# Kernel optimization log

Hardware: AMD Instinct MI355X
Metric: run time of the kernel (lower is better)

The kernel has to match this reference:

```python
import jax, jax.numpy as jnp
import numpy as np

B, T, C, H = 2, 2048, 1024, 16


def setup_inputs() -> dict:
    key = jax.random.key(0)
    ks = jax.random.split(key, 5)
    s = 0.02
    x = jax.random.normal(ks[0], (B, T, C), dtype=jnp.float32)
    # causal mask, shape [1, 1, T, T], 1 = attend, 0 = masked
    att_mask = jnp.tril(jnp.ones((T, T), dtype=jnp.int32))[None, None, :, :]
    w_kqv = jax.random.normal(ks[1], (C, 3 * C), dtype=jnp.float32) * s
    b_kqv = jax.random.normal(ks[2], (3 * C,), dtype=jnp.float32) * s
    w_proj = jax.random.normal(ks[3], (C, C), dtype=jnp.float32) * s
    b_proj = jax.random.normal(ks[4], (C,), dtype=jnp.float32) * s
    return {"x": x, "att_mask": att_mask, "w_kqv": w_kqv, "b_kqv": b_kqv,
            "w_proj": w_proj, "b_proj": b_proj, "n_head": H}


def reference(x, att_mask, w_kqv, b_kqv, w_proj, b_proj, n_head):
    b, t, c = x.shape
    hd = c // n_head
    # mixed kqv projection, then per-head chunks of 3*hd split as (k, q, v)
    kqv = (x @ w_kqv + b_kqv).reshape(b, t, n_head, 3 * hd)
    k, q, v = jnp.split(kqv, 3, axis=-1)            # each [b, t, h, hd]
    k = k.transpose(0, 2, 1, 3)                     # [b, h, t, hd]
    q = q.transpose(0, 2, 1, 3)
    v = v.transpose(0, 2, 1, 3)
    scale = 1.0 / np.sqrt(hd).astype(np.float32)
    att = jnp.einsum('bhqd,bhkd->bhqk', q, k) * scale
    att = jnp.where(att_mask[:, :, :t, :t] == 0, jnp.float32(-jnp.inf), att)
    att = jax.nn.softmax(att, axis=-1)
    y = jnp.einsum('bhqk,bhkd->bhqd', att, v)       # [b, h, t, hd]
    y = y.transpose(0, 2, 1, 3).reshape(b, t, c)
    return y @ w_proj + b_proj
```

## Files before the change

### kernel.cpp

```cpp
#include <hip/hip_runtime.h>
#include <hip/hip_bf16.h>

#define NB 2
#define NT 2048
#define NC 1024
#define NH 16
#define HD 64

typedef __attribute__((ext_vector_type(8))) short short8;
typedef __attribute__((ext_vector_type(4))) short short4_;
typedef __attribute__((ext_vector_type(4))) float f32x4;
typedef unsigned short u16;

__device__ __forceinline__ u16 f2bf(float x) {
  union { float f; unsigned u; } c; c.f = x;
  unsigned r = (c.u + 0x7fffu + ((c.u >> 16) & 1u)) >> 16;
  return (u16)r;
}


__global__ void cvt_x_kernel(const float* __restrict__ in, u16* __restrict__ out, int n) {
  int i = (blockIdx.x * blockDim.x + threadIdx.x) * 4;
  if (i < n) {
    float4 v = *(const float4*)(in + i);
    short4_ o;
    o.x = (short)f2bf(v.x); o.y = (short)f2bf(v.y);
    o.z = (short)f2bf(v.z); o.w = (short)f2bf(v.w);
    *(short4_*)(out + i) = o;
  }
}

__global__ void transpose_w_kernel(const float* __restrict__ in, u16* __restrict__ out,
                                   int K, int N) {
  __shared__ float tile[32][33];
  int k0 = blockIdx.x * 32, n0 = blockIdx.y * 32;
  int tx = threadIdx.x, ty = threadIdx.y;
  for (int r = ty; r < 32; r += 8)
    tile[r][tx] = in[(size_t)(k0 + r) * N + n0 + tx];
  __syncthreads();
  for (int r = ty; r < 32; r += 8)
    out[(size_t)(n0 + r) * K + k0 + tx] = f2bf(tile[tx][r]);
}


__global__ __launch_bounds__(256, 2) void gemm_kqv(
    const u16* __restrict__ A, const u16* __restrict__ Bt,
    const float* __restrict__ bias,
    u16* __restrict__ o_k, u16* __restrict__ o_q, u16* __restrict__ o_vt,
    int M, int N, int K) {
  __shared__ u16 As[128 * 32];
  __shared__ u16 Bs[128 * 32];
  __shared__ u16 Cs[128 * 128];
  int tid = threadIdx.x;
  int w = tid >> 6, l = tid & 63;
  int wr = w >> 1, wc = w & 1;
  int lr = l & 15, lk = l >> 4;
  int bm = blockIdx.x, bn = blockIdx.y;

  const u16* Ab = A + (size_t)bm * 128 * K;
  const u16* Bb = Bt + (size_t)bn * 128 * K;

  f32x4 acc[4][4];
#pragma unroll
  for (int m = 0; m < 4; m++)
#pragma unroll
    for (int n = 0; n < 4; n++) acc[m][n] = (f32x4){0.f, 0.f, 0.f, 0.f};

  for (int ks = 0; ks < K; ks += 32) {
    __syncthreads();
#pragma unroll
    for (int it = 0; it < 2; ++it) {
      int chunk = it * 256 + tid;
      int r = chunk >> 2, kg = chunk & 3;
      const u16* ga = Ab + (size_t)r * K + ks + kg * 8;
      const u16* gb = Bb + (size_t)r * K + ks + kg * 8;
      u16* la = As + (size_t)(it * 256 + w * 64) * 8;
      u16* lb = Bs + (size_t)(it * 256 + w * 64) * 8;
      __builtin_amdgcn_global_load_lds((const __attribute__((address_space(1))) void*)ga,
                                       (__attribute__((address_space(3))) void*)la, 16, 0, 0);
      __builtin_amdgcn_global_load_lds((const __attribute__((address_space(1))) void*)gb,
                                       (__attribute__((address_space(3))) void*)lb, 16, 0, 0);
    }
    __syncthreads();
    short8 a[4], b[4];
#pragma unroll
    for (int m = 0; m < 4; m++)
      a[m] = *(const short8*)(As + (size_t)(wr * 64 + m * 16 + lr) * 32 + lk * 8);
#pragma unroll
    for (int n = 0; n < 4; n++)
      b[n] = *(const short8*)(Bs + (size_t)(wc * 64 + n * 16 + lr) * 32 + lk * 8);
#pragma unroll
    for (int m = 0; m < 4; m++)
#pragma unroll
      for (int n = 0; n < 4; n++)
        acc[m][n] = __builtin_amdgcn_mfma_f32_16x16x32_bf16(a[m], b[n], acc[m][n], 0, 0, 0);
  }

#pragma unroll
  for (int n = 0; n < 4; n++) {
    int col = wc * 64 + n * 16 + lr;
    float bv = bias[bn * 128 + col];
#pragma unroll
    for (int m = 0; m < 4; m++) {
#pragma unroll
      for (int j = 0; j < 4; j++) {
        int row = wr * 64 + m * 16 + lk * 4 + j;
        int bo = (row * 256 + col * 2) ^ (((row >> 2) & 3) << 5);
        *(u16*)((char*)Cs + bo) = f2bf(acc[m][n][j] + bv);
      }
    }
  }
  __syncthreads();
#pragma unroll
  for (int i = 0; i < 8; i++) {
    int idx = i * 256 + tid;
    int row = idx >> 4, g = idx & 15;
    int gcol0 = bn * 128 + g * 8;
    unsigned head = (unsigned)gcol0 / 192u;
    int rem = gcol0 - (int)head * 192;
    int typ = rem >> 6, d0 = rem & 63;
    if (typ < 2) {
      int bo = (row * 256 + g * 16) ^ (((row >> 2) & 3) << 5);
      short8 val = *(const short8*)((const char*)Cs + bo);
      int grow = bm * 128 + row;
      int b_ = grow >> 11, t_ = grow & (NT - 1);
      size_t base = ((size_t)(b_ * NH + head) * NT + t_) * HD + d0;
      if (typ == 0) *(short8*)(o_k + base) = val;
      else          *(short8*)(o_q + base) = val;
    }
  }
  for (int i = tid; i < 128 * 16; i += 256) {
    int c = i >> 4, rg = i & 15;
    int gcol = bn * 128 + c;
    unsigned head = (unsigned)gcol / 192u;
    int rem = gcol - (int)head * 192;
    if (rem >= 128) {
      int d = rem - 128;
      short8 val;
#pragma unroll
      for (int k = 0; k < 8; k++) {
        int row = rg * 8 + k;
        int bo = (row * 256 + c * 2) ^ (((row >> 2) & 3) << 5);
        val[k] = *(const u16*)((const char*)Cs + bo);
      }
      int grow0 = bm * 128 + rg * 8;
      int b_ = grow0 >> 11, t0 = grow0 & (NT - 1);
      *(short8*)(o_vt + ((size_t)(b_ * NH + head) * HD + d) * NT + t0) = val;
    }
  }
}


__global__ __launch_bounds__(256, 2) void gemm_out(
    const u16* __restrict__ A, const u16* __restrict__ Bt,
    const float* __restrict__ bias, float* __restrict__ o_f, int M, int N, int K) {
  __shared__ u16 As[128 * 32];
  __shared__ u16 Bs[64 * 32];
  int tid = threadIdx.x;
  int w = tid >> 6, l = tid & 63;
  int wr = w >> 1, wc = w & 1;
  int lr = l & 15, lk = l >> 4;
  int bm = blockIdx.x, bn = blockIdx.y;

  const u16* Ab = A + (size_t)bm * 128 * K;
  const u16* Bb = Bt + (size_t)bn * 64 * K;

  f32x4 acc[4][2];
#pragma unroll
  for (int m = 0; m < 4; m++)
#pragma unroll
    for (int n = 0; n < 2; n++) acc[m][n] = (f32x4){0.f, 0.f, 0.f, 0.f};

  for (int ks = 0; ks < K; ks += 32) {
    __syncthreads();
#pragma unroll
    for (int it = 0; it < 2; ++it) {
      int chunk = it * 256 + tid;
      int r = chunk >> 2, kg = chunk & 3;
      const u16* ga = Ab + (size_t)r * K + ks + kg * 8;
      u16* la = As + (size_t)(it * 256 + w * 64) * 8;
      __builtin_amdgcn_global_load_lds((const __attribute__((address_space(1))) void*)ga,
                                       (__attribute__((address_space(3))) void*)la, 16, 0, 0);
    }
    {
      int r = tid >> 2, kg = tid & 3;
      const u16* gb = Bb + (size_t)r * K + ks + kg * 8;
      u16* lb = Bs + (size_t)(w * 64) * 8;
      __builtin_amdgcn_global_load_lds((const __attribute__((address_space(1))) void*)gb,
                                       (__attribute__((address_space(3))) void*)lb, 16, 0, 0);
    }
    __syncthreads();
    short8 a[4], b[2];
#pragma unroll
    for (int m = 0; m < 4; m++)
      a[m] = *(const short8*)(As + (size_t)(wr * 64 + m * 16 + lr) * 32 + lk * 8);
#pragma unroll
    for (int n = 0; n < 2; n++)
      b[n] = *(const short8*)(Bs + (size_t)(wc * 32 + n * 16 + lr) * 32 + lk * 8);
#pragma unroll
    for (int m = 0; m < 4; m++)
#pragma unroll
      for (int n = 0; n < 2; n++)
        acc[m][n] = __builtin_amdgcn_mfma_f32_16x16x32_bf16(a[m], b[n], acc[m][n], 0, 0, 0);
  }

#pragma unroll
  for (int m = 0; m < 4; m++) {
    int gm0 = bm * 128 + wr * 64 + m * 16 + lk * 4;
#pragma unroll
    for (int n = 0; n < 2; n++) {
      int gn = bn * 64 + wc * 32 + n * 16 + lr;
      float bv = bias[gn];
#pragma unroll
      for (int j = 0; j < 4; j++)
        o_f[(size_t)(gm0 + j) * N + gn] = acc[m][n][j] + bv;
    }
  }
}


#define SMSCALE 0.1803368801111137f
#define FIXSHIFT 8.0f

__device__ __forceinline__ void stage_kv(const u16* __restrict__ Kp, const u16* __restrict__ Vp,
                                         u16* Ksb, u16* Vsb, int kt, int tid, int w) {
#pragma unroll
  for (int i = 0; i < 2; i++) {
    int o = i * 4096 + tid * 16;
    int row = o >> 7, b = o & 127;
    int sb = b ^ ((row & 7) << 4);
    const char* gk = (const char*)Kp + (size_t)(kt * 64 + row) * 128 + sb;
    const char* gv = (const char*)Vp + (size_t)row * (NT * 2) + (size_t)kt * 128 + sb;
    u16* lk = Ksb + (i * 4096 + w * 1024) / 2;
    u16* lv = Vsb + (i * 4096 + w * 1024) / 2;
    __builtin_amdgcn_global_load_lds((const __attribute__((address_space(1))) void*)gk,
                                     (__attribute__((address_space(3))) void*)lk, 16, 0, 0);
    __builtin_amdgcn_global_load_lds((const __attribute__((address_space(1))) void*)gv,
                                     (__attribute__((address_space(3))) void*)lv, 16, 0, 0);
  }
}

template <bool LAST>
__device__ __forceinline__ void attn_step(
    const u16* __restrict__ Kl, const u16* __restrict__ Vl, u16* __restrict__ Pw,
    const short8 (&qf)[2], f32x4 (&accO)[4],
    float& lsum, int mtmax, int kv0, int qg, int lr, int lg) {
  int swm = (lr & 7) << 4;
  float p[4][4];
#pragma unroll
  for (int mt = 0; mt < 4; ++mt) {
    bool act = !LAST || (mt < mtmax);
    if (act) {
      f32x4 a = (f32x4){0.f, 0.f, 0.f, 0.f};
#pragma unroll
      for (int c = 0; c < 2; c++) {
        int rk = mt * 16 + lr;
        short8 kf = *(const short8*)((const char*)Kl + rk * 128 + ((c * 64 + lg * 16) ^ swm));
        a = __builtin_amdgcn_mfma_f32_16x16x32_bf16(kf, qf[c], a, 0, 0, 0);
      }
#pragma unroll
      for (int j = 0; j < 4; j++) {
        float v = __builtin_fmaf(a[j], SMSCALE, -FIXSHIFT);
        if (LAST) {
          int kvg = kv0 + mt * 16 + lg * 4 + j;
          v = (kvg <= qg) ? v : -1e30f;
        }
        p[mt][j] = exp2f(v);
      }
    } else {
#pragma unroll
      for (int j = 0; j < 4; j++) p[mt][j] = 0.f;
    }
  }
#pragma unroll
  for (int mt = 0; mt < 4; mt++)
#pragma unroll
    for (int j = 0; j < 4; j++) lsum += p[mt][j];

#pragma unroll
  for (int mt = 0; mt < 4; mt++) {
    union { __hip_bfloat162 h[2]; uint2 u; } pk;
    pk.h[0] = __float22bfloat162_rn(make_float2(p[mt][0], p[mt][1]));
    pk.h[1] = __float22bfloat162_rn(make_float2(p[mt][2], p[mt][3]));
    int bo = (lr * 128 + mt * 32 + lg * 8) ^ swm;
    *(uint2*)((char*)Pw + bo) = pk.u;
  }
#pragma unroll
  for (int c = 0; c < 2; c++) {
    int bo = (lr * 128 + c * 64 + lg * 16) ^ swm;
    short8 pa = *(const short8*)((const char*)Pw + bo);
#pragma unroll
    for (int n = 0; n < 4; n++) {
      int rv = n * 16 + lr;
      short8 vf = *(const short8*)((const char*)Vl + rv * 128 + ((c * 64 + lg * 16) ^ swm));
      accO[n] = __builtin_amdgcn_mfma_f32_16x16x32_bf16(pa, vf, accO[n], 0, 0, 0);
    }
  }
}

__global__ __launch_bounds__(256, 4) void attn_kernel(
    const u16* __restrict__ Kb, const u16* __restrict__ Qb,
    const u16* __restrict__ Vt, u16* __restrict__ Y) {
  int id = blockIdx.x;
  int xcd = id & 7, idx = id >> 3;
  int bh = xcd * 4 + (idx & 3);
  int qb = 31 - (idx >> 2);

  int tid = threadIdx.x;
  int w = tid >> 6, l = tid & 63;
  int lr = l & 15, lg = l >> 4;
  int q0 = qb * 64 + w * 16;

  const u16* Kp = Kb + (size_t)bh * NT * HD;
  const u16* Qp = Qb + (size_t)bh * NT * HD;
  const u16* Vp = Vt + (size_t)bh * HD * NT;

  __shared__ u16 Ks[2][64 * 64];
  __shared__ u16 Vs[2][64 * 64];
  __shared__ u16 Pl[4][16 * 64];
  u16* Pw = &Pl[w][0];

  short8 qf[2];
#pragma unroll
  for (int c = 0; c < 2; c++)
    qf[c] = *(const short8*)(Qp + (size_t)(q0 + lr) * HD + c * 32 + lg * 8);

  f32x4 accO[4];
#pragma unroll
  for (int n = 0; n < 4; n++) accO[n] = (f32x4){0.f, 0.f, 0.f, 0.f};
  float lsum = 0.f;
  int qg = q0 + lr;
  int nt = qb + 1;

  stage_kv(Kp, Vp, Ks[0], Vs[0], 0, tid, w);
  __syncthreads();

  for (int kt = 0; kt < nt - 1; ++kt) {
    int cur = kt & 1;
    stage_kv(Kp, Vp, Ks[cur ^ 1], Vs[cur ^ 1], kt + 1, tid, w);
    attn_step<false>(Ks[cur], Vs[cur], Pw, qf, accO, lsum, 4, kt * 64, qg, lr, lg);
    __syncthreads();
  }
  {
    int cur = (nt - 1) & 1;
    attn_step<true>(Ks[cur], Vs[cur], Pw, qf, accO, lsum, w + 1, (nt - 1) * 64, qg, lr, lg);
  }

  lsum += __shfl_xor(lsum, 16);
  lsum += __shfl_xor(lsum, 32);
  float rl[4];
#pragma unroll
  for (int j = 0; j < 4; j++) rl[j] = 1.0f / __shfl(lsum, lg * 4 + j);
  int b_ = bh >> 4, h_ = bh & 15;
#pragma unroll
  for (int n = 0; n < 4; n++)
#pragma unroll
    for (int j = 0; j < 4; j++) {
      int q = q0 + lg * 4 + j;
      Y[((size_t)(b_ * NT + q)) * NC + h_ * HD + n * 16 + lr] = f2bf(accO[n][j] * rl[j]);
    }
}


extern "C" void kernel_launch(void* const* d_in, const int* in_sizes, int n_in,
                              void* d_out, int out_size, void* d_ws, size_t ws_size,
                              hipStream_t stream) {
  const float* x      = (const float*)d_in[0];
  const float* w_kqv  = (const float*)d_in[2];
  const float* b_kqv  = (const float*)d_in[3];
  const float* w_proj = (const float*)d_in[4];
  const float* b_proj = (const float*)d_in[5];
  float* out = (float*)d_out;

  const size_t M = (size_t)NB * NT;
  u16* xb     = (u16*)d_ws;
  u16* wkqvT  = xb + M * NC;
  u16* wprojT = wkqvT + (size_t)3 * NC * NC;
  u16* Kb     = wprojT + (size_t)NC * NC;
  u16* Qb     = Kb + M * NC;
  u16* Vt     = Qb + M * NC;
  u16* Yb     = Vt + M * NC;

  int nx = (int)(M * NC);
  cvt_x_kernel<<<nx / (256 * 4), 256, 0, stream>>>(x, xb, nx);
  dim3 tb(32, 8);
  transpose_w_kernel<<<dim3(NC / 32, 3 * NC / 32), tb, 0, stream>>>(w_kqv, wkqvT, NC, 3 * NC);
  transpose_w_kernel<<<dim3(NC / 32, NC / 32), tb, 0, stream>>>(w_proj, wprojT, NC, NC);

  gemm_kqv<<<dim3(32, 24), 256, 0, stream>>>(xb, wkqvT, b_kqv, Kb, Qb, Vt,
                                             (int)M, 3 * NC, NC);
  attn_kernel<<<1024, 256, 0, stream>>>(Kb, Qb, Vt, Yb);
  gemm_out<<<dim3(32, 16), 256, 0, stream>>>(Yb, wprojT, b_proj, out, (int)M, NC, NC);
}
```

Before: 201.4 us.

## Process two query tiles per attention block to reuse staged K/V tiles

Each attention block now handles 128 query rows as two 64-row groups, spaced 64 apart, that share every K/V tile staged in LDS. This halves the grid and the K/V global-to-LDS traffic per query. Causal work is balanced by pairing query blocks in a zigzag order. The inner step is restructured to pre-offset the LDS pointers, wrap the MFMA clusters in s_setprio, and split the final diagonal tiles into two masked modes. The cost is more registers per wave (occupancy hint lowered from 4 to 3) and a coarser grid of 512 blocks.

```diff
diff --git a/kernel.cpp b/kernel.cpp
--- a/kernel.cpp
+++ b/kernel.cpp
@@ -222,94 +222,90 @@
 #define SMSCALE 0.1803368801111137f
 #define FIXSHIFT 8.0f
 
-__device__ __forceinline__ void stage_kv(const u16* __restrict__ Kp, const u16* __restrict__ Vp,
-                                         u16* Ksb, u16* Vsb, int kt, int tid, int w) {
-#pragma unroll
-  for (int i = 0; i < 2; i++) {
-    int o = i * 4096 + tid * 16;
-    int row = o >> 7, b = o & 127;
-    int sb = b ^ ((row & 7) << 4);
-    const char* gk = (const char*)Kp + (size_t)(kt * 64 + row) * 128 + sb;
-    const char* gv = (const char*)Vp + (size_t)row * (NT * 2) + (size_t)kt * 128 + sb;
-    u16* lk = Ksb + (i * 4096 + w * 1024) / 2;
-    u16* lv = Vsb + (i * 4096 + w * 1024) / 2;
-    __builtin_amdgcn_global_load_lds((const __attribute__((address_space(1))) void*)gk,
-                                     (__attribute__((address_space(3))) void*)lk, 16, 0, 0);
-    __builtin_amdgcn_global_load_lds((const __attribute__((address_space(1))) void*)gv,
-                                     (__attribute__((address_space(3))) void*)lv, 16, 0, 0);
-  }
-}
-
-template <bool LAST>
+template <int MODE>
 __device__ __forceinline__ void attn_step(
-    const u16* __restrict__ Kl, const u16* __restrict__ Vl, u16* __restrict__ Pw,
-    const short8 (&qf)[2], f32x4 (&accO)[4],
-    float& lsum, int mtmax, int kv0, int qg, int lr, int lg) {
-  int swm = (lr & 7) << 4;
-  float p[4][4];
+    const char* __restrict__ Kl, const char* __restrict__ Vl,
+    u16* __restrict__ Pw0, u16* __restrict__ Pw1,
+    const short8 (&qf)[2][2], f32x4 (&acc0)[4], f32x4 (&acc1)[4],
+    float& ls0, float& ls1, int kv0, int qg0, int qg1, int lr, int lg, int swm) {
+  const char* KlC0 = Kl + lr * 128 + ((lg * 16) ^ swm);
+  const char* KlC1 = Kl + lr * 128 + ((64 + lg * 16) ^ swm);
+  float p0[4][4], p1[4][4];
 #pragma unroll
   for (int mt = 0; mt < 4; ++mt) {
-    bool act = !LAST || (mt < mtmax);
-    if (act) {
-      f32x4 a = (f32x4){0.f, 0.f, 0.f, 0.f};
-#pragma unroll
-      for (int c = 0; c < 2; c++) {
-        int rk = mt * 16 + lr;
-        short8 kf = *(const short8*)((const char*)Kl + rk * 128 + ((c * 64 + lg * 16) ^ swm));
-        a = __builtin_amdgcn_mfma_f32_16x16x32_bf16(kf, qf[c], a, 0, 0, 0);
+    short8 kf0 = *(const short8*)(KlC0 + mt * 2048);
+    short8 kf1 = *(const short8*)(KlC1 + mt * 2048);
+    f32x4 a0 = (f32x4){0.f, 0.f, 0.f, 0.f}, a1 = a0;
+    __builtin_amdgcn_s_setprio(1);
+    if (MODE != 2) {
+      a0 = __builtin_amdgcn_mfma_f32_16x16x32_bf16(kf0, qf[0][0], a0, 0, 0, 0);
+      a0 = __builtin_amdgcn_mfma_f32_16x16x32_bf16(kf1, qf[0][1], a0, 0, 0, 0);
+    }
+    a1 = __builtin_amdgcn_mfma_f32_16x16x32_bf16(kf0, qf[1][0], a1, 0, 0, 0);
+    a1 = __builtin_amdgcn_mfma_f32_16x16x32_bf16(kf1, qf[1][1], a1, 0, 0, 0);
+    __builtin_amdgcn_s_setprio(0);
+#pragma unroll
+    for (int j = 0; j < 4; j++) {
+      int kvg = kv0 + mt * 16 + lg * 4 + j;
+      if (MODE != 2) {
+        float v = __builtin_fmaf(a0[j], SMSCALE, -FIXSHIFT);
+        if (MODE == 1) v = (kvg <= qg0) ? v : -1e30f;
+        float p = exp2f(v);
+        p0[mt][j] = p; ls0 += p;
       }
-#pragma unroll
-      for (int j = 0; j < 4; j++) {
-        float v = __builtin_fmaf(a[j], SMSCALE, -FIXSHIFT);
-        if (LAST) {
-          int kvg = kv0 + mt * 16 + lg * 4 + j;
-          v = (kvg <= qg) ? v : -1e30f;
-        }
-        p[mt][j] = exp2f(v);
+      {
+        float v = __builtin_fmaf(a1[j], SMSCALE, -FIXSHIFT);
+        if (MODE == 2) v = (kvg <= qg1) ? v : -1e30f;
+        float p = exp2f(v);
+        p1[mt][j] = p; ls1 += p;
       }
-    } else {
-#pragma unroll
-      for (int j = 0; j < 4; j++) p[mt][j] = 0.f;
-    }
-  }
-#pragma unroll
-  for (int mt = 0; mt < 4; mt++)
-#pragma unroll
-    for (int j = 0; j < 4; j++) lsum += p[mt][j];
-
+    }
+  }
 #pragma unroll
   for (int mt = 0; mt < 4; mt++) {
+    int bo = (lr * 128 + mt * 32 + lg * 8) ^ swm;
+    if (MODE != 2) {
+      union { __hip_bfloat162 h[2]; uint2 u; } pk;
+      pk.h[0] = __float22bfloat162_rn(make_float2(p0[mt][0], p0[mt][1]));
+      pk.h[1] = __float22bfloat162_rn(make_float2(p0[mt][2], p0[mt][3]));
+      *(uint2*)((char*)Pw0 + bo) = pk.u;
+    }
     union { __hip_bfloat162 h[2]; uint2 u; } pk;
-    pk.h[0] = __float22bfloat162_rn(make_float2(p[mt][0], p[mt][1]));
-    pk.h[1] = __float22bfloat162_rn(make_float2(p[mt][2], p[mt][3]));
-    int bo = (lr * 128 + mt * 32 + lg * 8) ^ swm;
-    *(uint2*)((char*)Pw + bo) = pk.u;
+    pk.h[0] = __float22bfloat162_rn(make_float2(p1[mt][0], p1[mt][1]));
+    pk.h[1] = __float22bfloat162_rn(make_float2(p1[mt][2], p1[mt][3]));
+    *(uint2*)((char*)Pw1 + bo) = pk.u;
   }
 #pragma unroll
   for (int c = 0; c < 2; c++) {
     int bo = (lr * 128 + c * 64 + lg * 16) ^ swm;
-    short8 pa = *(const short8*)((const char*)Pw + bo);
+    short8 pa0, pa1;
+    if (MODE != 2) pa0 = *(const short8*)((const char*)Pw0 + bo);
+    pa1 = *(const short8*)((const char*)Pw1 + bo);
+    const char* VlC = Vl + lr * 128 + ((c * 64 + lg * 16) ^ swm);
+    __builtin_amdgcn_s_setprio(1);
 #pragma unroll
     for (int n = 0; n < 4; n++) {
-      int rv = n * 16 + lr;
-      short8 vf = *(const short8*)((const char*)Vl + rv * 128 + ((c * 64 + lg * 16) ^ swm));
-      accO[n] = __builtin_amdgcn_mfma_f32_16x16x32_bf16(pa, vf, accO[n], 0, 0, 0);
-    }
-  }
-}
-
-__global__ __launch_bounds__(256, 4) void attn_kernel(
+      short8 vf = *(const short8*)(VlC + n * 2048);
+      if (MODE != 2) acc0[n] = __builtin_amdgcn_mfma_f32_16x16x32_bf16(pa0, vf, acc0[n], 0, 0, 0);
+      acc1[n] = __builtin_amdgcn_mfma_f32_16x16x32_bf16(pa1, vf, acc1[n], 0, 0, 0);
+    }
+    __builtin_amdgcn_s_setprio(0);
+  }
+}
+
+__global__ __launch_bounds__(256, 3) void attn_kernel(
     const u16* __restrict__ Kb, const u16* __restrict__ Qb,
     const u16* __restrict__ Vt, u16* __restrict__ Y) {
   int id = blockIdx.x;
   int xcd = id & 7, idx = id >> 3;
   int bh = xcd * 4 + (idx & 3);
-  int qb = 31 - (idx >> 2);
+  int qbo = idx >> 2;
+  int qb = (qbo < 8) ? (15 - 2 * qbo) : (2 * (qbo - 8));
 
   int tid = threadIdx.x;
   int w = tid >> 6, l = tid & 63;
   int lr = l & 15, lg = l >> 4;
-  int q0 = qb * 64 + w * 16;
+  int swm = (lr & 7) << 4;
 
   const u16* Kp = Kb + (size_t)bh * NT * HD;
   const u16* Qp = Qb + (size_t)bh * NT * HD;
@@ -317,48 +313,89 @@
 
   __shared__ u16 Ks[2][64 * 64];
   __shared__ u16 Vs[2][64 * 64];
-  __shared__ u16 Pl[4][16 * 64];
-  u16* Pw = &Pl[w][0];
-
-  short8 qf[2];
-#pragma unroll
-  for (int c = 0; c < 2; c++)
-    qf[c] = *(const short8*)(Qp + (size_t)(q0 + lr) * HD + c * 32 + lg * 8);
-
-  f32x4 accO[4];
-#pragma unroll
-  for (int n = 0; n < 4; n++) accO[n] = (f32x4){0.f, 0.f, 0.f, 0.f};
-  float lsum = 0.f;
-  int qg = q0 + lr;
-  int nt = qb + 1;
-
-  stage_kv(Kp, Vp, Ks[0], Vs[0], 0, tid, w);
+  __shared__ u16 Pl[4][2][1024];
+  u16* Pw0 = &Pl[w][0][0];
+  u16* Pw1 = &Pl[w][1][0];
+
+  int q00 = qb * 128 + w * 16;
+  int q01 = q00 + 64;
+  short8 qf[2][2];
+#pragma unroll
+  for (int g = 0; g < 2; g++)
+#pragma unroll
+    for (int c = 0; c < 2; c++)
+      qf[g][c] = *(const short8*)(Qp + (size_t)(q00 + g * 64 + lr) * HD + c * 32 + lg * 8);
+
+  f32x4 acc0[4], acc1[4];
+#pragma unroll
+  for (int n = 0; n < 4; n++) { acc0[n] = (f32x4){0.f, 0.f, 0.f, 0.f}; acc1[n] = acc0[n]; }
+  float ls0 = 0.f, ls1 = 0.f;
+  int qg0 = q00 + lr, qg1 = q01 + lr;
+
+  int o = tid * 16;
+  int srow = o >> 7, sb = (o & 127) ^ ((srow & 7) << 4);
+  const char* gk = (const char*)Kp + (size_t)srow * 128 + sb;
+  const char* gv = (const char*)Vp + (size_t)srow * (NT * 2) + sb;
+  char* kd0 = (char*)&Ks[0][0] + w * 1024;
+  char* kd1 = (char*)&Ks[1][0] + w * 1024;
+  char* vd0 = (char*)&Vs[0][0] + w * 1024;
+  char* vd1 = (char*)&Vs[1][0] + w * 1024;
+
+#define STAGE(KD, VD)                                                                         \
+  do {                                                                                        \
+    __builtin_amdgcn_global_load_lds((const __attribute__((address_space(1))) void*)gk,       \
+                                     (__attribute__((address_space(3))) void*)(KD), 16, 0, 0);\
+    __builtin_amdgcn_global_load_lds((const __attribute__((address_space(1))) void*)(gk+4096),\
+                                     (__attribute__((address_space(3))) void*)((KD)+4096), 16, 0, 0);\
+    __builtin_amdgcn_global_load_lds((const __attribute__((address_space(1))) void*)gv,       \
+                                     (__attribute__((address_space(3))) void*)(VD), 16, 0, 0);\
+    __builtin_amdgcn_global_load_lds((const __attribute__((address_space(1))) void*)(gv+32*4096),\
+                                     (__attribute__((address_space(3))) void*)((VD)+4096), 16, 0, 0);\
+    gk += 8192; gv += 128;                                                                    \
+  } while (0)
+
+  STAGE(kd0, vd0);
   __syncthreads();
 
-  for (int kt = 0; kt < nt - 1; ++kt) {
-    int cur = kt & 1;
-    stage_kv(Kp, Vp, Ks[cur ^ 1], Vs[cur ^ 1], kt + 1, tid, w);
-    attn_step<false>(Ks[cur], Vs[cur], Pw, qf, accO, lsum, 4, kt * 64, qg, lr, lg);
+  int nfull = 2 * qb;
+  for (int kt = 0; kt < nfull; ++kt) {
+    if (kt & 1) {
+      STAGE(kd0, vd0);
+      attn_step<0>((const char*)&Ks[1][0], (const char*)&Vs[1][0], Pw0, Pw1, qf,
+                   acc0, acc1, ls0, ls1, kt * 64, qg0, qg1, lr, lg, swm);
+    } else {
+      STAGE(kd1, vd1);
+      attn_step<0>((const char*)&Ks[0][0], (const char*)&Vs[0][0], Pw0, Pw1, qf,
+                   acc0, acc1, ls0, ls1, kt * 64, qg0, qg1, lr, lg, swm);
+    }
     __syncthreads();
   }
-  {
-    int cur = (nt - 1) & 1;
-    attn_step<true>(Ks[cur], Vs[cur], Pw, qf, accO, lsum, w + 1, (nt - 1) * 64, qg, lr, lg);
-  }
-
-  lsum += __shfl_xor(lsum, 16);
-  lsum += __shfl_xor(lsum, 32);
-  float rl[4];
-#pragma unroll
-  for (int j = 0; j < 4; j++) rl[j] = 1.0f / __shfl(lsum, lg * 4 + j);
+  STAGE(kd1, vd1);
+  attn_step<1>((const char*)&Ks[0][0], (const char*)&Vs[0][0], Pw0, Pw1, qf,
+               acc0, acc1, ls0, ls1, nfull * 64, qg0, qg1, lr, lg, swm);
+  __syncthreads();
+  attn_step<2>((const char*)&Ks[1][0], (const char*)&Vs[1][0], Pw0, Pw1, qf,
+               acc0, acc1, ls0, ls1, (nfull + 1) * 64, qg0, qg1, lr, lg, swm);
+#undef STAGE
+
+  ls0 += __shfl_xor(ls0, 16); ls0 += __shfl_xor(ls0, 32);
+  ls1 += __shfl_xor(ls1, 16); ls1 += __shfl_xor(ls1, 32);
   int b_ = bh >> 4, h_ = bh & 15;
 #pragma unroll
-  for (int n = 0; n < 4; n++)
-#pragma unroll
-    for (int j = 0; j < 4; j++) {
-      int q = q0 + lg * 4 + j;
-      Y[((size_t)(b_ * NT + q)) * NC + h_ * HD + n * 16 + lr] = f2bf(accO[n][j] * rl[j]);
-    }
+  for (int g = 0; g < 2; g++) {
+    float lsg = g ? ls1 : ls0;
+    float rl[4];
+#pragma unroll
+    for (int j = 0; j < 4; j++) rl[j] = 1.0f / __shfl(lsg, lg * 4 + j);
+#pragma unroll
+    for (int n = 0; n < 4; n++)
+#pragma unroll
+      for (int j = 0; j < 4; j++) {
+        int q = q00 + g * 64 + lg * 4 + j;
+        float v = (g ? acc1[n][j] : acc0[n][j]) * rl[j];
+        Y[((size_t)(b_ * NT + q)) * NC + h_ * HD + n * 16 + lr] = f2bf(v);
+      }
+  }
 }
 
 
@@ -389,6 +426,6 @@
 
   gemm_kqv<<<dim3(32, 24), 256, 0, stream>>>(xb, wkqvT, b_kqv, Kb, Qb, Vt,
                                              (int)M, 3 * NC, NC);
-  attn_kernel<<<1024, 256, 0, stream>>>(Kb, Qb, Vt, Yb);
+  attn_kernel<<<512, 256, 0, stream>>>(Kb, Qb, Vt, Yb);
   gemm_out<<<dim3(32, 16), 256, 0, stream>>>(Yb, wprojT, b_proj, out, (int)M, NC, NC);
 }
```

After: 210.0 us. 1.04x slower.

## Double GEMM k-tile to 64 with XOR-swizzled LDS and aliased epilogue buffer

Applied to the files above, without the earlier changes.

Both GEMMs now stage 64-wide k-slices per iteration instead of 32, with an XOR swizzle on the 16-byte chunks so that reading MFMA fragments from LDS avoids bank conflicts. This halves the number of barrier pairs per GEMM. In gemm_kqv the output staging buffer now shares memory with the A/B tiles, keeping LDS at 32KB so occupancy can rise to 3 blocks per CU. The two weight-transpose launches are merged into one kernel to drop a launch. The cost is more registers and LDS per k-step and an extra barrier before the epilogue.

```diff
diff --git a/kernel.cpp b/kernel.cpp
--- a/kernel.cpp
+++ b/kernel.cpp
@@ -11,6 +11,10 @@
 typedef __attribute__((ext_vector_type(4))) short short4_;
 typedef __attribute__((ext_vector_type(4))) float f32x4;
 typedef unsigned short u16;
+
+#define GLOAD16(G, L)                                                                   \
+  __builtin_amdgcn_global_load_lds((const __attribute__((address_space(1))) void*)(G),  \
+                                   (__attribute__((address_space(3))) void*)(L), 16, 0, 0)
 
 __device__ __forceinline__ u16 f2bf(float x) {
   union { float f; unsigned u; } c; c.f = x;
@@ -30,35 +34,40 @@
   }
 }
 
-__global__ void transpose_w_kernel(const float* __restrict__ in, u16* __restrict__ out,
-                                   int K, int N) {
+__global__ void transpose_w2_kernel(const float* __restrict__ wk, u16* __restrict__ ok,
+                                    const float* __restrict__ wp, u16* __restrict__ op) {
   __shared__ float tile[32][33];
-  int k0 = blockIdx.x * 32, n0 = blockIdx.y * 32;
+  int by = blockIdx.y;
+  const float* in; u16* out; int N, n0;
+  if (by < 96) { in = wk; out = ok; N = 3072; n0 = by * 32; }
+  else         { in = wp; out = op; N = 1024; n0 = (by - 96) * 32; }
+  int k0 = blockIdx.x * 32;
   int tx = threadIdx.x, ty = threadIdx.y;
   for (int r = ty; r < 32; r += 8)
     tile[r][tx] = in[(size_t)(k0 + r) * N + n0 + tx];
   __syncthreads();
   for (int r = ty; r < 32; r += 8)
-    out[(size_t)(n0 + r) * K + k0 + tx] = f2bf(tile[tx][r]);
-}
-
-
-__global__ __launch_bounds__(256, 2) void gemm_kqv(
+    out[(size_t)(n0 + r) * NC + k0 + tx] = f2bf(tile[tx][r]);
+}
+
+
+__global__ __launch_bounds__(256, 3) void gemm_kqv(
     const u16* __restrict__ A, const u16* __restrict__ Bt,
     const float* __restrict__ bias,
     u16* __restrict__ o_k, u16* __restrict__ o_q, u16* __restrict__ o_vt,
     int M, int N, int K) {
-  __shared__ u16 As[128 * 32];
-  __shared__ u16 Bs[128 * 32];
-  __shared__ u16 Cs[128 * 128];
+  __shared__ char smem[32768];
+  u16* Cs = (u16*)smem;
+  char* As = smem;
+  char* Bs = smem + 16384;
   int tid = threadIdx.x;
   int w = tid >> 6, l = tid & 63;
   int wr = w >> 1, wc = w & 1;
   int lr = l & 15, lk = l >> 4;
   int bm = blockIdx.x, bn = blockIdx.y;
 
-  const u16* Ab = A + (size_t)bm * 128 * K;
-  const u16* Bb = Bt + (size_t)bn * 128 * K;
+  const char* Ab = (const char*)(A + (size_t)bm * 128 * K);
+  const char* Bb = (const char*)(Bt + (size_t)bn * 128 * K);
 
   f32x4 acc[4][4];
 #pragma unroll
@@ -66,35 +75,37 @@
 #pragma unroll
     for (int n = 0; n < 4; n++) acc[m][n] = (f32x4){0.f, 0.f, 0.f, 0.f};
 
-  for (int ks = 0; ks < K; ks += 32) {
+  for (int ks = 0; ks < K; ks += 64) {
     __syncthreads();
 #pragma unroll
-    for (int it = 0; it < 2; ++it) {
+    for (int it = 0; it < 4; ++it) {
       int chunk = it * 256 + tid;
-      int r = chunk >> 2, kg = chunk & 3;
-      const u16* ga = Ab + (size_t)r * K + ks + kg * 8;
-      const u16* gb = Bb + (size_t)r * K + ks + kg * 8;
-      u16* la = As + (size_t)(it * 256 + w * 64) * 8;
-      u16* lb = Bs + (size_t)(it * 256 + w * 64) * 8;
-      __builtin_amdgcn_global_load_lds((const __attribute__((address_space(1))) void*)ga,
-                                       (__attribute__((address_space(3))) void*)la, 16, 0, 0);
-      __builtin_amdgcn_global_load_lds((const __attribute__((address_space(1))) void*)gb,
-                                       (__attribute__((address_space(3))) void*)lb, 16, 0, 0);
+      int r = chunk >> 3, c16 = chunk & 7;
+      int sb = (c16 << 4) ^ ((r & 7) << 4);
+      const char* ga = Ab + (size_t)r * (K * 2) + ks * 2 + sb;
+      const char* gb = Bb + (size_t)r * (K * 2) + ks * 2 + sb;
+      GLOAD16(ga, As + (it * 256 + w * 64) * 16);
+      GLOAD16(gb, Bs + (it * 256 + w * 64) * 16);
     }
     __syncthreads();
-    short8 a[4], b[4];
-#pragma unroll
-    for (int m = 0; m < 4; m++)
-      a[m] = *(const short8*)(As + (size_t)(wr * 64 + m * 16 + lr) * 32 + lk * 8);
-#pragma unroll
-    for (int n = 0; n < 4; n++)
-      b[n] = *(const short8*)(Bs + (size_t)(wc * 64 + n * 16 + lr) * 32 + lk * 8);
-#pragma unroll
-    for (int m = 0; m < 4; m++)
+#pragma unroll
+    for (int kk = 0; kk < 2; ++kk) {
+      int co = (kk * 64 + lk * 16) ^ ((lr & 7) << 4);
+      short8 a[4], b[4];
+#pragma unroll
+      for (int m = 0; m < 4; m++)
+        a[m] = *(const short8*)(As + (wr * 64 + m * 16 + lr) * 128 + co);
 #pragma unroll
       for (int n = 0; n < 4; n++)
-        acc[m][n] = __builtin_amdgcn_mfma_f32_16x16x32_bf16(a[m], b[n], acc[m][n], 0, 0, 0);
-  }
+        b[n] = *(const short8*)(Bs + (wc * 64 + n * 16 + lr) * 128 + co);
+#pragma unroll
+      for (int m = 0; m < 4; m++)
+#pragma unroll
+        for (int n = 0; n < 4; n++)
+          acc[m][n] = __builtin_amdgcn_mfma_f32_16x16x32_bf16(a[m], b[n], acc[m][n], 0, 0, 0);
+    }
+  }
+  __syncthreads();
 
 #pragma unroll
   for (int n = 0; n < 4; n++) {
@@ -154,16 +165,16 @@
 __global__ __launch_bounds__(256, 2) void gemm_out(
     const u16* __restrict__ A, const u16* __restrict__ Bt,
     const float* __restrict__ bias, float* __restrict__ o_f, int M, int N, int K) {
-  __shared__ u16 As[128 * 32];
-  __shared__ u16 Bs[64 * 32];
+  __shared__ char As[128 * 128];
+  __shared__ char Bs[64 * 128];
   int tid = threadIdx.x;
   int w = tid >> 6, l = tid & 63;
   int wr = w >> 1, wc = w & 1;
   int lr = l & 15, lk = l >> 4;
   int bm = blockIdx.x, bn = blockIdx.y;
 
-  const u16* Ab = A + (size_t)bm * 128 * K;
-  const u16* Bb = Bt + (size_t)bn * 64 * K;
+  const char* Ab = (const char*)(A + (size_t)bm * 128 * K);
+  const char* Bb = (const char*)(Bt + (size_t)bn * 64 * K);
 
   f32x4 acc[4][2];
 #pragma unroll
@@ -171,37 +182,39 @@
 #pragma unroll
     for (int n = 0; n < 2; n++) acc[m][n] = (f32x4){0.f, 0.f, 0.f, 0.f};
 
-  for (int ks = 0; ks < K; ks += 32) {
+  for (int ks = 0; ks < K; ks += 64) {
     __syncthreads();
+#pragma unroll
+    for (int it = 0; it < 4; ++it) {
+      int chunk = it * 256 + tid;
+      int r = chunk >> 3, c16 = chunk & 7;
+      int sb = (c16 << 4) ^ ((r & 7) << 4);
+      GLOAD16(Ab + (size_t)r * (K * 2) + ks * 2 + sb, As + (it * 256 + w * 64) * 16);
+    }
 #pragma unroll
     for (int it = 0; it < 2; ++it) {
       int chunk = it * 256 + tid;
-      int r = chunk >> 2, kg = chunk & 3;
-      const u16* ga = Ab + (size_t)r * K + ks + kg * 8;
-      u16* la = As + (size_t)(it * 256 + w * 64) * 8;
-      __builtin_amdgcn_global_load_lds((const __attribute__((address_space(1))) void*)ga,
-                                       (__attribute__((address_space(3))) void*)la, 16, 0, 0);
-    }
-    {
-      int r = tid >> 2, kg = tid & 3;
-      const u16* gb = Bb + (size_t)r * K + ks + kg * 8;
-      u16* lb = Bs + (size_t)(w * 64) * 8;
-      __builtin_amdgcn_global_load_lds((const __attribute__((address_space(1))) void*)gb,
-                                       (__attribute__((address_space(3))) void*)lb, 16, 0, 0);
+      int r = chunk >> 3, c16 = chunk & 7;
+      int sb = (c16 << 4) ^ ((r & 7) << 4);
+      GLOAD16(Bb + (size_t)r * (K * 2) + ks * 2 + sb, Bs + (it * 256 + w * 64) * 16);
     }
     __syncthreads();
-    short8 a[4], b[2];
-#pragma unroll
-    for (int m = 0; m < 4; m++)
-      a[m] = *(const short8*)(As + (size_t)(wr * 64 + m * 16 + lr) * 32 + lk * 8);
-#pragma unroll
-    for (int n = 0; n < 2; n++)
-      b[n] = *(const short8*)(Bs + (size_t)(wc * 32 + n * 16 + lr) * 32 + lk * 8);
-#pragma unroll
-    for (int m = 0; m < 4; m++)
+#pragma unroll
+    for (int kk = 0; kk < 2; ++kk) {
+      int co = (kk * 64 + lk * 16) ^ ((lr & 7) << 4);
+      short8 a[4], b[2];
+#pragma unroll
+      for (int m = 0; m < 4; m++)
+        a[m] = *(const short8*)(As + (wr * 64 + m * 16 + lr) * 128 + co);
 #pragma unroll
       for (int n = 0; n < 2; n++)
-        acc[m][n] = __builtin_amdgcn_mfma_f32_16x16x32_bf16(a[m], b[n], acc[m][n], 0, 0, 0);
+        b[n] = *(const short8*)(Bs + (wc * 32 + n * 16 + lr) * 128 + co);
+#pragma unroll
+      for (int m = 0; m < 4; m++)
+#pragma unroll
+        for (int n = 0; n < 2; n++)
+          acc[m][n] = __builtin_amdgcn_mfma_f32_16x16x32_bf16(a[m], b[n], acc[m][n], 0, 0, 0);
+    }
   }
 
 #pragma unroll
@@ -233,10 +246,8 @@
     const char* gv = (const char*)Vp + (size_t)row * (NT * 2) + (size_t)kt * 128 + sb;
     u16* lk = Ksb + (i * 4096 + w * 1024) / 2;
     u16* lv = Vsb + (i * 4096 + w * 1024) / 2;
-    __builtin_amdgcn_global_load_lds((const __attribute__((address_space(1))) void*)gk,
-                                     (__attribute__((address_space(3))) void*)lk, 16, 0, 0);
-    __builtin_amdgcn_global_load_lds((const __attribute__((address_space(1))) void*)gv,
-                                     (__attribute__((address_space(3))) void*)lv, 16, 0, 0);
+    GLOAD16(gk, lk);
+    GLOAD16(gv, lv);
   }
 }
 
@@ -383,9 +394,7 @@
 
   int nx = (int)(M * NC);
   cvt_x_kernel<<<nx / (256 * 4), 256, 0, stream>>>(x, xb, nx);
-  dim3 tb(32, 8);
-  transpose_w_kernel<<<dim3(NC / 32, 3 * NC / 32), tb, 0, stream>>>(w_kqv, wkqvT, NC, 3 * NC);
-  transpose_w_kernel<<<dim3(NC / 32, NC / 32), tb, 0, stream>>>(w_proj, wprojT, NC, NC);
+  transpose_w2_kernel<<<dim3(32, 128), dim3(32, 8), 0, stream>>>(w_kqv, wkqvT, w_proj, wprojT);
 
   gemm_kqv<<<dim3(32, 24), 256, 0, stream>>>(xb, wkqvT, b_kqv, Kb, Qb, Vt,
                                              (int)M, 3 * NC, NC);
```

After: 191.3 us. 5.0% less time.
